# Kernel optimization log

Hardware: AMD Instinct MI355X
Metric: run time of the kernel (lower is better)

## Reference

```python
import jax, jax.numpy as jnp
import numpy as np

B, T, H = 2048, 784, 64
STATE_DIM = 1
IN_DIM = 1 + STATE_DIM  # concat([t, y])
INNER_LR = 0.01
NUM_GRAD_STEPS = 4


def _unif(k, shape, fan_in):
    lim = 1.0 / np.sqrt(fan_in)
    return jax.random.uniform(k, shape, jnp.float32, -lim, lim)


def setup_inputs() -> dict:
    key = jax.random.key(0)
    ks = jax.random.split(key, 8)
    ts = (jnp.arange(T, dtype=jnp.float32) / T)
    xs = jax.random.normal(ks[0], (B, T), jnp.float32)
    mask = jax.random.bernoulli(ks[1], 0.5, (B, T - 1))  # teacher-forcing draws
    # equinox Linear default init: U(-1/sqrt(fan_in), 1/sqrt(fan_in)) for W and b
    W1 = _unif(ks[2], (H, IN_DIM), IN_DIM)
    b1 = _unif(ks[3], (H,), IN_DIM)
    W2 = _unif(ks[4], (H, H), H)
    b2 = _unif(ks[5], (H,), H)
    W3 = _unif(ks[6], (STATE_DIM, H), H)
    b3 = _unif(ks[7], (STATE_DIM,), H)
    return {"ts": ts, "xs": xs, "mask": mask,
            "W1": W1, "b1": b1, "W2": W2, "b2": b2, "W3": W3, "b3": b3}


def _mlp(theta, t, y):
    # theta: tuple of (W1,b1,W2,b2,W3,b3); t, y scalars -> output (state_dim,)
    W1, b1, W2, b2, W3, b3 = theta
    h = jnp.stack([t, y])                # (2,)
    h = jnp.tanh(W1 @ h + b1)            # (H,)
    h = jnp.tanh(W2 @ h + b2)            # (H,)
    return W3 @ h + b3                   # (state_dim,)


def reference(ts, xs, mask, W1, b1, W2, b2, W3, b3):
    theta0 = (W1, b1, W2, b2, W3, b3)

    def forward(xs_row, mask_row):
        def step(carry, inp):
            theta, t_prev, x_hat, x_prev = carry
            x_true, t_curr, m = inp
            x_t = jnp.where(m, x_true, x_hat)  # bernoulli(0.5) teacher forcing

            def inner_loss(th):
                pred = _mlp(th, t_curr, x_prev)
                return jnp.mean((pred - x_t) ** 2)

            for _ in range(NUM_GRAD_STEPS):
                g = jax.grad(inner_loss)(theta)
                theta = jax.tree_util.tree_map(
                    lambda p, gr: p - INNER_LR * gr, theta, g)

            deltat = t_curr - t_prev
            x_hat_new = _mlp(theta, t_curr + deltat, x_true).squeeze()
            return (theta, t_curr, x_hat_new, x_true), x_hat_new

        init = (theta0, ts[0], xs_row[0], xs_row[0])
        _, x_hats = jax.lax.scan(step, init, (xs_row[1:], ts[1:], mask_row))
        return jnp.concatenate([xs_row[:1], x_hats], axis=0)  # (T,)

    return jax.vmap(forward)(xs, mask)  # (B, T)
```

## Files before the change

### kernel.cpp

```cpp
#include <hip/hip_runtime.h>
#include <math.h>


#define TT  784
#define HH  64
#define LR  0.01f

typedef _Float16 h2v __attribute__((ext_vector_type(2)));
#define FDOT2(a, b, c) __builtin_amdgcn_fdot2((a), (b), (c), false)
#define BC(f) __builtin_bit_cast(h2v, (f))
#define PKFMA(acc, a, b) acc = __builtin_elementwise_fma((a), (b), (acc))

__device__ __forceinline__ float fast_tanh(float x) {
    float e = __builtin_amdgcn_exp2f(x * 2.885390081777926814f);
    float r = __builtin_amdgcn_rcpf(e + 1.0f);
    return fmaf(-2.0f, r, 1.0f);
}

template <int CTRL, int RMASK, bool BC_>
__device__ __forceinline__ float dpp_add(float x) {
    int t = __builtin_amdgcn_update_dpp(0, __builtin_bit_cast(int, x),
                                        CTRL, RMASK, 0xf, BC_);
    return x + __builtin_bit_cast(float, t);
}

__device__ __forceinline__ float wave_sum(float x) {
    x = dpp_add<0x111, 0xf, true>(x);
    x = dpp_add<0x112, 0xf, true>(x);
    x = dpp_add<0x114, 0xf, true>(x);
    x = dpp_add<0x118, 0xf, true>(x);
    x = dpp_add<0x142, 0xa, false>(x);
    x = dpp_add<0x143, 0xc, false>(x);
    return __builtin_bit_cast(float,
        __builtin_amdgcn_readlane(__builtin_bit_cast(int, x), 63));
}

__global__ __launch_bounds__(64, 2)
void ttt_kernel(const float* __restrict__ ts,
                const float* __restrict__ xs,
                const int*   __restrict__ mask,
                const float* __restrict__ W1,
                const float* __restrict__ b1,
                const float* __restrict__ W2,
                const float* __restrict__ b2,
                const float* __restrict__ W3,
                const float* __restrict__ b3,
                float* __restrict__ out)
{
    __shared__ __align__(16) _Float16 s_h1h[HH];
    __shared__ __align__(16) _Float16 s_uh[HH];
    __shared__ float s_ts[TT];
    __shared__ float s_xs[TT];
    __shared__ float s_out[TT];
    __shared__ int   s_mask[TT - 1];

    const int row  = blockIdx.x;
    const int lane = threadIdx.x;

    for (int i = lane; i < TT; i += HH) {
        s_ts[i] = ts[i];
        s_xs[i] = xs[row * TT + i];
    }
    for (int i = lane; i < TT - 1; i += HH) s_mask[i] = mask[row * (TT - 1) + i];

    float w1a = W1[2 * lane + 0];
    float w1b = W1[2 * lane + 1];
    float b1v = b1[lane];
    float b2v = b2[lane];
    float w3v = W3[lane];
    float b3v = b3[0];

    h2v w2r[HH / 2];
    h2v w2c[HH / 2];
#pragma unroll
    for (int k = 0; k < HH / 2; ++k) {
        w2r[k] = h2v{(_Float16)W2[lane * HH + 2 * k], (_Float16)W2[lane * HH + 2 * k + 1]};
        w2c[k] = h2v{(_Float16)W2[(2 * k) * HH + lane], (_Float16)W2[(2 * k + 1) * HH + lane]};
    }
    __syncthreads();

    const float4* h1v4 = (const float4*)s_h1h;
    const float4* uv4  = (const float4*)s_uh;

    float t_prev = s_ts[0];
    const float x0 = s_xs[0];
    float x_hat  = x0;
    float x_prev = x0;
    if (lane == 0) s_out[0] = x0;

    float4 hr[8];
    float  h1f, h2f, predf;
    float  ul;
    float  z1f;
    float  sdz1 = 0.f;
    float  tc = 0.f, x_true = 0.f, tin = 0.f, nls = 0.f;

    auto MERGED = [&](float xt, bool final_) {
        const float diff = predf - xt;
        const float dl   = diff + diff;
        const float ndl  = -LR * dl;
        w3v = fmaf(ndl, h2f, w3v);
        b3v += ndl;
        b2v = fmaf(ndl, ul, b2v);
        const _Float16 sd = (_Float16)(ndl * ul);
        const h2v sdv = h2v{sd, sd};
        const _Float16 sh = (_Float16)(ndl * h1f);
        const h2v shv = h2v{sh, sh};
        float d0 = 0.f, d1 = 0.f, d2 = 0.f, d3 = 0.f;
#pragma unroll
        for (int k = 0; k < 8; ++k) {
            float4 q = uv4[k];
            d0 = FDOT2(w2c[4 * k + 0], BC(q.x), d0);
            d1 = FDOT2(w2c[4 * k + 1], BC(q.y), d1);
            d2 = FDOT2(w2c[4 * k + 2], BC(q.z), d2);
            d3 = FDOT2(w2c[4 * k + 3], BC(q.w), d3);
            PKFMA(w2c[4 * k + 0], shv, BC(q.x));
            PKFMA(w2c[4 * k + 1], shv, BC(q.y));
            PKFMA(w2c[4 * k + 2], shv, BC(q.z));
            PKFMA(w2c[4 * k + 3], shv, BC(q.w));
        }
        const float raw = (d0 + d1) + (d2 + d3);
        const float dh1 = dl * raw;
        const float dz1 = dh1 * fmaf(-h1f, h1f, 1.0f);
        sdz1 += dz1;
        if (!final_) {
            z1f = fmaf(nls, dz1, z1f);
        } else {
            w1a = fmaf(-LR * tc,     sdz1, w1a);
            w1b = fmaf(-LR * x_prev, sdz1, w1b);
            b1v = fmaf(-LR,          sdz1, b1v);
            z1f = fmaf(w1a, tin, fmaf(w1b, x_true, b1v));
        }
        h1f = fast_tanh(z1f);
        s_h1h[lane] = (_Float16)h1f;
#pragma unroll
        for (int k = 0; k < 8; ++k) {
            float4 o = hr[k];
            PKFMA(w2r[4 * k + 0], sdv, BC(o.x));
            PKFMA(w2r[4 * k + 1], sdv, BC(o.y));
            PKFMA(w2r[4 * k + 2], sdv, BC(o.z));
            PKFMA(w2r[4 * k + 3], sdv, BC(o.w));
        }
        float a0 = b2v, a1 = 0.f, a2 = 0.f, a3 = 0.f;
#pragma unroll
        for (int k = 0; k < 8; ++k) {
            float4 q = h1v4[k];
            hr[k] = q;
            a0 = FDOT2(w2r[4 * k + 0], BC(q.x), a0);
            a1 = FDOT2(w2r[4 * k + 1], BC(q.y), a1);
            a2 = FDOT2(w2r[4 * k + 2], BC(q.z), a2);
            a3 = FDOT2(w2r[4 * k + 3], BC(q.w), a3);
        }
        const float z2 = (a0 + a1) + (a2 + a3);
        h2f = fast_tanh(z2);
        const float uf = w3v * fmaf(-h2f, h2f, 1.0f);
        ul = uf;
        s_uh[lane] = (_Float16)uf;
        predf = wave_sum(w3v * h2f) + b3v;
    };

    z1f = fmaf(w1a, s_ts[1], fmaf(w1b, x0, b1v));
    h1f = fast_tanh(z1f);
    s_h1h[lane] = (_Float16)h1f;
    {
        float a0 = b2v, a1 = 0.f, a2 = 0.f, a3 = 0.f;
#pragma unroll
        for (int k = 0; k < 8; ++k) {
            float4 q = h1v4[k];
            hr[k] = q;
            a0 = FDOT2(w2r[4 * k + 0], BC(q.x), a0);
            a1 = FDOT2(w2r[4 * k + 1], BC(q.y), a1);
            a2 = FDOT2(w2r[4 * k + 2], BC(q.z), a2);
            a3 = FDOT2(w2r[4 * k + 3], BC(q.w), a3);
        }
        const float z2 = (a0 + a1) + (a2 + a3);
        h2f = fast_tanh(z2);
        const float uf = w3v * fmaf(-h2f, h2f, 1.0f);
        ul = uf;
        s_uh[lane] = (_Float16)uf;
        predf = wave_sum(w3v * h2f) + b3v;
    }

    for (int t = 1; t < TT; ++t) {
        tc     = s_ts[t];
        x_true = s_xs[t];
        tin    = tc + (tc - t_prev);
        nls    = -LR * fmaf(tc, tc, fmaf(x_prev, x_prev, 1.0f));
        const float x_t = s_mask[t - 1] ? x_true : x_hat;

        sdz1 = 0.f;
        MERGED(x_t, false);
        MERGED(x_t, false);
        MERGED(x_t, false);
        MERGED(x_t, true);
        x_hat = predf;

        if (lane == 0) s_out[t] = x_hat;
        t_prev = tc;
        x_prev = x_true;
    }

    for (int i = lane; i < TT; i += HH) out[row * TT + i] = s_out[i];
}

extern "C" void kernel_launch(void* const* d_in, const int* in_sizes, int n_in,
                              void* d_out, int out_size, void* d_ws, size_t ws_size,
                              hipStream_t stream) {
    const float* ts   = (const float*)d_in[0];
    const float* xs   = (const float*)d_in[1];
    const int*   mask = (const int*)d_in[2];
    const float* W1   = (const float*)d_in[3];
    const float* b1   = (const float*)d_in[4];
    const float* W2   = (const float*)d_in[5];
    const float* b2   = (const float*)d_in[6];
    const float* W3   = (const float*)d_in[7];
    const float* b3   = (const float*)d_in[8];
    float* out = (float*)d_out;

    const int B = in_sizes[1] / TT;
    dim3 grid(B), block(HH);
    hipLaunchKernelGGL(ttt_kernel, grid, block, 0, stream,
                       ts, xs, mask, W1, b1, W2, b2, W3, b3, out);
}
```

Baseline: 2.518 ms.

## Broadcast hidden vectors via DPP and readlane instead of LDS round-trips

Replaces the shared-memory staging of the fp16 h1 and u vectors with a DPP lane shift that packs neighbouring halves, followed by 32 readlanes into scalar/uniform registers. This removes LDS writes, reads and the implicit wait on them from the serial per-step dependency chain. It also folds the subtraction of x_t into the wave reduction by pre-dividing the bias term by 64, and splits the dot products into eight accumulators for more ILP. The cost is 64 readlane instructions per inner step and slightly different rounding in the loss gradient.

```diff
diff --git a/kernel.cpp b/kernel.cpp
--- a/kernel.cpp
+++ b/kernel.cpp
@@ -8,7 +8,7 @@
 
 typedef _Float16 h2v __attribute__((ext_vector_type(2)));
 #define FDOT2(a, b, c) __builtin_amdgcn_fdot2((a), (b), (c), false)
-#define BC(f) __builtin_bit_cast(h2v, (f))
+#define BCI(i) __builtin_bit_cast(h2v, (i))
 #define PKFMA(acc, a, b) acc = __builtin_elementwise_fma((a), (b), (acc))
 
 __device__ __forceinline__ float fast_tanh(float x) {
@@ -33,6 +33,10 @@
     x = dpp_add<0x143, 0xc, false>(x);
     return __builtin_bit_cast(float,
         __builtin_amdgcn_readlane(__builtin_bit_cast(int, x), 63));
+}
+
+__device__ __forceinline__ int lane_shl1(int v) {
+    return __builtin_amdgcn_update_dpp(0, v, 0x101, 0xf, 0xf, false);
 }
 
 __global__ __launch_bounds__(64, 2)
@@ -47,8 +51,6 @@
                 const float* __restrict__ b3,
                 float* __restrict__ out)
 {
-    __shared__ __align__(16) _Float16 s_h1h[HH];
-    __shared__ __align__(16) _Float16 s_uh[HH];
     __shared__ float s_ts[TT];
     __shared__ float s_xs[TT];
     __shared__ float s_out[TT];
@@ -79,26 +81,32 @@
     }
     __syncthreads();
 
-    const float4* h1v4 = (const float4*)s_h1h;
-    const float4* uv4  = (const float4*)s_uh;
-
     float t_prev = s_ts[0];
     const float x0 = s_xs[0];
     float x_hat  = x0;
     float x_prev = x0;
     if (lane == 0) s_out[0] = x0;
 
-    float4 hr[8];
+    int hb[32];
+    int ub[32];
     float  h1f, h2f, predf;
     float  ul;
     float  z1f;
     float  sdz1 = 0.f;
     float  tc = 0.f, x_true = 0.f, tin = 0.f, nls = 0.f;
 
-    auto MERGED = [&](float xt, bool final_) {
-        const float diff = predf - xt;
-        const float dl   = diff + diff;
-        const float ndl  = -LR * dl;
+    auto GATHER = [&](float x, int* dst) {
+        const int lo = (int)__builtin_bit_cast(unsigned short, (_Float16)x);
+        const int nb = lane_shl1(lo);
+        const int pk = lo | (nb << 16);
+#pragma unroll
+        for (int k = 0; k < 32; ++k)
+            dst[k] = __builtin_amdgcn_readlane(pk, 2 * k);
+    };
+
+    auto MERGED = [&](float diff, float xt, bool final_) -> float {
+        const float k12 = -2.0f * fmaf(h1f, h1f, -1.0f);
+        const float ndl = diff * (-2.0f * LR);
         w3v = fmaf(ndl, h2f, w3v);
         b3v += ndl;
         b2v = fmaf(ndl, ul, b2v);
@@ -107,21 +115,30 @@
         const _Float16 sh = (_Float16)(ndl * h1f);
         const h2v shv = h2v{sh, sh};
         float d0 = 0.f, d1 = 0.f, d2 = 0.f, d3 = 0.f;
+        float d4 = 0.f, d5 = 0.f, d6 = 0.f, d7 = 0.f;
 #pragma unroll
         for (int k = 0; k < 8; ++k) {
-            float4 q = uv4[k];
-            d0 = FDOT2(w2c[4 * k + 0], BC(q.x), d0);
-            d1 = FDOT2(w2c[4 * k + 1], BC(q.y), d1);
-            d2 = FDOT2(w2c[4 * k + 2], BC(q.z), d2);
-            d3 = FDOT2(w2c[4 * k + 3], BC(q.w), d3);
-            PKFMA(w2c[4 * k + 0], shv, BC(q.x));
-            PKFMA(w2c[4 * k + 1], shv, BC(q.y));
-            PKFMA(w2c[4 * k + 2], shv, BC(q.z));
-            PKFMA(w2c[4 * k + 3], shv, BC(q.w));
-        }
-        const float raw = (d0 + d1) + (d2 + d3);
-        const float dh1 = dl * raw;
-        const float dz1 = dh1 * fmaf(-h1f, h1f, 1.0f);
+            const h2v q0 = BCI(ub[4 * k + 0]), q1 = BCI(ub[4 * k + 1]);
+            const h2v q2 = BCI(ub[4 * k + 2]), q3 = BCI(ub[4 * k + 3]);
+            if (k & 1) {
+                d4 = FDOT2(w2c[4 * k + 0], q0, d4);
+                d5 = FDOT2(w2c[4 * k + 1], q1, d5);
+                d6 = FDOT2(w2c[4 * k + 2], q2, d6);
+                d7 = FDOT2(w2c[4 * k + 3], q3, d7);
+            } else {
+                d0 = FDOT2(w2c[4 * k + 0], q0, d0);
+                d1 = FDOT2(w2c[4 * k + 1], q1, d1);
+                d2 = FDOT2(w2c[4 * k + 2], q2, d2);
+                d3 = FDOT2(w2c[4 * k + 3], q3, d3);
+            }
+            PKFMA(w2c[4 * k + 0], shv, q0);
+            PKFMA(w2c[4 * k + 1], shv, q1);
+            PKFMA(w2c[4 * k + 2], shv, q2);
+            PKFMA(w2c[4 * k + 3], shv, q3);
+        }
+        const float raw = ((d0 + d4) + (d1 + d5)) + ((d2 + d6) + (d3 + d7));
+        const float rk2 = raw * k12;
+        const float dz1 = diff * rk2;
         sdz1 += dz1;
         if (!final_) {
             z1f = fmaf(nls, dz1, z1f);
@@ -132,53 +149,64 @@
             z1f = fmaf(w1a, tin, fmaf(w1b, x_true, b1v));
         }
         h1f = fast_tanh(z1f);
-        s_h1h[lane] = (_Float16)h1f;
+#pragma unroll
+        for (int k = 0; k < 32; ++k) PKFMA(w2r[k], sdv, BCI(hb[k]));
+        GATHER(h1f, hb);
+        float a0 = b2v, a1 = 0.f, a2 = 0.f, a3 = 0.f;
+        float a4 = 0.f, a5 = 0.f, a6 = 0.f, a7 = 0.f;
 #pragma unroll
         for (int k = 0; k < 8; ++k) {
-            float4 o = hr[k];
-            PKFMA(w2r[4 * k + 0], sdv, BC(o.x));
-            PKFMA(w2r[4 * k + 1], sdv, BC(o.y));
-            PKFMA(w2r[4 * k + 2], sdv, BC(o.z));
-            PKFMA(w2r[4 * k + 3], sdv, BC(o.w));
-        }
-        float a0 = b2v, a1 = 0.f, a2 = 0.f, a3 = 0.f;
-#pragma unroll
-        for (int k = 0; k < 8; ++k) {
-            float4 q = h1v4[k];
-            hr[k] = q;
-            a0 = FDOT2(w2r[4 * k + 0], BC(q.x), a0);
-            a1 = FDOT2(w2r[4 * k + 1], BC(q.y), a1);
-            a2 = FDOT2(w2r[4 * k + 2], BC(q.z), a2);
-            a3 = FDOT2(w2r[4 * k + 3], BC(q.w), a3);
-        }
-        const float z2 = (a0 + a1) + (a2 + a3);
+            const h2v q0 = BCI(hb[4 * k + 0]), q1 = BCI(hb[4 * k + 1]);
+            const h2v q2 = BCI(hb[4 * k + 2]), q3 = BCI(hb[4 * k + 3]);
+            if (k & 1) {
+                a4 = FDOT2(w2r[4 * k + 0], q0, a4);
+                a5 = FDOT2(w2r[4 * k + 1], q1, a5);
+                a6 = FDOT2(w2r[4 * k + 2], q2, a6);
+                a7 = FDOT2(w2r[4 * k + 3], q3, a7);
+            } else {
+                a0 = FDOT2(w2r[4 * k + 0], q0, a0);
+                a1 = FDOT2(w2r[4 * k + 1], q1, a1);
+                a2 = FDOT2(w2r[4 * k + 2], q2, a2);
+                a3 = FDOT2(w2r[4 * k + 3], q3, a3);
+            }
+        }
+        const float z2 = ((a0 + a4) + (a1 + a5)) + ((a2 + a6) + (a3 + a7));
         h2f = fast_tanh(z2);
         const float uf = w3v * fmaf(-h2f, h2f, 1.0f);
         ul = uf;
-        s_uh[lane] = (_Float16)uf;
-        predf = wave_sum(w3v * h2f) + b3v;
+        GATHER(uf, ub);
+        const float cadd = (final_ ? b3v : (b3v - xt)) * 0.015625f;
+        return wave_sum(fmaf(w3v, h2f, cadd));
     };
 
     z1f = fmaf(w1a, s_ts[1], fmaf(w1b, x0, b1v));
     h1f = fast_tanh(z1f);
-    s_h1h[lane] = (_Float16)h1f;
+    GATHER(h1f, hb);
     {
         float a0 = b2v, a1 = 0.f, a2 = 0.f, a3 = 0.f;
+        float a4 = 0.f, a5 = 0.f, a6 = 0.f, a7 = 0.f;
 #pragma unroll
         for (int k = 0; k < 8; ++k) {
-            float4 q = h1v4[k];
-            hr[k] = q;
-            a0 = FDOT2(w2r[4 * k + 0], BC(q.x), a0);
-            a1 = FDOT2(w2r[4 * k + 1], BC(q.y), a1);
-            a2 = FDOT2(w2r[4 * k + 2], BC(q.z), a2);
-            a3 = FDOT2(w2r[4 * k + 3], BC(q.w), a3);
-        }
-        const float z2 = (a0 + a1) + (a2 + a3);
+            const h2v q0 = BCI(hb[4 * k + 0]), q1 = BCI(hb[4 * k + 1]);
+            const h2v q2 = BCI(hb[4 * k + 2]), q3 = BCI(hb[4 * k + 3]);
+            if (k & 1) {
+                a4 = FDOT2(w2r[4 * k + 0], q0, a4);
+                a5 = FDOT2(w2r[4 * k + 1], q1, a5);
+                a6 = FDOT2(w2r[4 * k + 2], q2, a6);
+                a7 = FDOT2(w2r[4 * k + 3], q3, a7);
+            } else {
+                a0 = FDOT2(w2r[4 * k + 0], q0, a0);
+                a1 = FDOT2(w2r[4 * k + 1], q1, a1);
+                a2 = FDOT2(w2r[4 * k + 2], q2, a2);
+                a3 = FDOT2(w2r[4 * k + 3], q3, a3);
+            }
+        }
+        const float z2 = ((a0 + a4) + (a1 + a5)) + ((a2 + a6) + (a3 + a7));
         h2f = fast_tanh(z2);
         const float uf = w3v * fmaf(-h2f, h2f, 1.0f);
         ul = uf;
-        s_uh[lane] = (_Float16)uf;
-        predf = wave_sum(w3v * h2f) + b3v;
+        GATHER(uf, ub);
+        predf = wave_sum(fmaf(w3v, h2f, b3v * 0.015625f));
     }
 
     for (int t = 1; t < TT; ++t) {
@@ -189,10 +217,11 @@
         const float x_t = s_mask[t - 1] ? x_true : x_hat;
 
         sdz1 = 0.f;
-        MERGED(x_t, false);
-        MERGED(x_t, false);
-        MERGED(x_t, false);
-        MERGED(x_t, true);
+        float df = predf - x_t;
+        df    = MERGED(df, x_t, false);
+        df    = MERGED(df, x_t, false);
+        df    = MERGED(df, x_t, false);
+        predf = MERGED(df, x_t, true);
         x_hat = predf;
 
         if (lane == 0) s_out[t] = x_hat;
```

Result: slower. 3.244 ms (+28.8%).

## Switch W2 state from packed fp16 to fp32 with double-buffered LDS activations

Applied to the files above, without the earlier changes.

Replaces the packed half-precision W2 registers, fdot2 and packed-FMA updates with full fp32 weights and scalar FMAs. It also double-buffers the h1 activations in shared memory instead of caching the old h1 in registers for the rank-1 update. This roughly doubles the register footprint for W2 (128 floats per lane) and doubles the ALU instruction count in the inner loops. In exchange it removes fp16 rounding drift in the weights over many steps, with added risk of register spilling or lower occupancy.

```diff
diff --git a/kernel.cpp b/kernel.cpp
--- a/kernel.cpp
+++ b/kernel.cpp
@@ -5,11 +5,6 @@
 #define TT  784
 #define HH  64
 #define LR  0.01f
-
-typedef _Float16 h2v __attribute__((ext_vector_type(2)));
-#define FDOT2(a, b, c) __builtin_amdgcn_fdot2((a), (b), (c), false)
-#define BC(f) __builtin_bit_cast(h2v, (f))
-#define PKFMA(acc, a, b) acc = __builtin_elementwise_fma((a), (b), (acc))
 
 __device__ __forceinline__ float fast_tanh(float x) {
     float e = __builtin_amdgcn_exp2f(x * 2.885390081777926814f);
@@ -47,8 +42,8 @@
                 const float* __restrict__ b3,
                 float* __restrict__ out)
 {
-    __shared__ __align__(16) _Float16 s_h1h[HH];
-    __shared__ __align__(16) _Float16 s_uh[HH];
+    __shared__ __align__(16) float s_hb[2][HH];
+    __shared__ __align__(16) float s_ub[HH];
     __shared__ float s_ts[TT];
     __shared__ float s_xs[TT];
     __shared__ float s_out[TT];
@@ -70,17 +65,18 @@
     float w3v = W3[lane];
     float b3v = b3[0];
 
-    h2v w2r[HH / 2];
-    h2v w2c[HH / 2];
-#pragma unroll
-    for (int k = 0; k < HH / 2; ++k) {
-        w2r[k] = h2v{(_Float16)W2[lane * HH + 2 * k], (_Float16)W2[lane * HH + 2 * k + 1]};
-        w2c[k] = h2v{(_Float16)W2[(2 * k) * HH + lane], (_Float16)W2[(2 * k + 1) * HH + lane]};
+    float w2r[HH];
+    float w2c[HH];
+#pragma unroll
+    for (int j = 0; j < HH; ++j) {
+        w2r[j] = W2[lane * HH + j];
+        w2c[j] = W2[j * HH + lane];
     }
     __syncthreads();
 
-    const float4* h1v4 = (const float4*)s_h1h;
-    const float4* uv4  = (const float4*)s_uh;
+    const float4* hb0 = (const float4*)s_hb[0];
+    const float4* hb1 = (const float4*)s_hb[1];
+    const float4* ub4 = (const float4*)s_ub;
 
     float t_prev = s_ts[0];
     const float x0 = s_xs[0];
@@ -88,36 +84,34 @@
     float x_prev = x0;
     if (lane == 0) s_out[0] = x0;
 
-    float4 hr[8];
     float  h1f, h2f, predf;
     float  ul;
     float  z1f;
     float  sdz1 = 0.f;
     float  tc = 0.f, x_true = 0.f, tin = 0.f, nls = 0.f;
 
-    auto MERGED = [&](float xt, bool final_) {
+    auto MERGED = [&](const float4* hold, const float4* hnew, float* hst,
+                      float xt, bool final_) {
         const float diff = predf - xt;
         const float dl   = diff + diff;
         const float ndl  = -LR * dl;
         w3v = fmaf(ndl, h2f, w3v);
         b3v += ndl;
         b2v = fmaf(ndl, ul, b2v);
-        const _Float16 sd = (_Float16)(ndl * ul);
-        const h2v sdv = h2v{sd, sd};
-        const _Float16 sh = (_Float16)(ndl * h1f);
-        const h2v shv = h2v{sh, sh};
+        const float sd = ndl * ul;
+        const float sh = ndl * h1f;
         float d0 = 0.f, d1 = 0.f, d2 = 0.f, d3 = 0.f;
 #pragma unroll
-        for (int k = 0; k < 8; ++k) {
-            float4 q = uv4[k];
-            d0 = FDOT2(w2c[4 * k + 0], BC(q.x), d0);
-            d1 = FDOT2(w2c[4 * k + 1], BC(q.y), d1);
-            d2 = FDOT2(w2c[4 * k + 2], BC(q.z), d2);
-            d3 = FDOT2(w2c[4 * k + 3], BC(q.w), d3);
-            PKFMA(w2c[4 * k + 0], shv, BC(q.x));
-            PKFMA(w2c[4 * k + 1], shv, BC(q.y));
-            PKFMA(w2c[4 * k + 2], shv, BC(q.z));
-            PKFMA(w2c[4 * k + 3], shv, BC(q.w));
+        for (int k = 0; k < 16; ++k) {
+            const float4 q = ub4[k];
+            d0 = fmaf(w2c[4 * k + 0], q.x, d0);
+            d1 = fmaf(w2c[4 * k + 1], q.y, d1);
+            d2 = fmaf(w2c[4 * k + 2], q.z, d2);
+            d3 = fmaf(w2c[4 * k + 3], q.w, d3);
+            w2c[4 * k + 0] = fmaf(sh, q.x, w2c[4 * k + 0]);
+            w2c[4 * k + 1] = fmaf(sh, q.y, w2c[4 * k + 1]);
+            w2c[4 * k + 2] = fmaf(sh, q.z, w2c[4 * k + 2]);
+            w2c[4 * k + 3] = fmaf(sh, q.w, w2c[4 * k + 3]);
         }
         const float raw = (d0 + d1) + (d2 + d3);
         const float dh1 = dl * raw;
@@ -132,52 +126,47 @@
             z1f = fmaf(w1a, tin, fmaf(w1b, x_true, b1v));
         }
         h1f = fast_tanh(z1f);
-        s_h1h[lane] = (_Float16)h1f;
-#pragma unroll
-        for (int k = 0; k < 8; ++k) {
-            float4 o = hr[k];
-            PKFMA(w2r[4 * k + 0], sdv, BC(o.x));
-            PKFMA(w2r[4 * k + 1], sdv, BC(o.y));
-            PKFMA(w2r[4 * k + 2], sdv, BC(o.z));
-            PKFMA(w2r[4 * k + 3], sdv, BC(o.w));
-        }
+        hst[lane] = h1f;
         float a0 = b2v, a1 = 0.f, a2 = 0.f, a3 = 0.f;
 #pragma unroll
-        for (int k = 0; k < 8; ++k) {
-            float4 q = h1v4[k];
-            hr[k] = q;
-            a0 = FDOT2(w2r[4 * k + 0], BC(q.x), a0);
-            a1 = FDOT2(w2r[4 * k + 1], BC(q.y), a1);
-            a2 = FDOT2(w2r[4 * k + 2], BC(q.z), a2);
-            a3 = FDOT2(w2r[4 * k + 3], BC(q.w), a3);
+        for (int k = 0; k < 16; ++k) {
+            const float4 qo = hold[k];
+            w2r[4 * k + 0] = fmaf(sd, qo.x, w2r[4 * k + 0]);
+            w2r[4 * k + 1] = fmaf(sd, qo.y, w2r[4 * k + 1]);
+            w2r[4 * k + 2] = fmaf(sd, qo.z, w2r[4 * k + 2]);
+            w2r[4 * k + 3] = fmaf(sd, qo.w, w2r[4 * k + 3]);
+            const float4 qn = hnew[k];
+            a0 = fmaf(w2r[4 * k + 0], qn.x, a0);
+            a1 = fmaf(w2r[4 * k + 1], qn.y, a1);
+            a2 = fmaf(w2r[4 * k + 2], qn.z, a2);
+            a3 = fmaf(w2r[4 * k + 3], qn.w, a3);
         }
         const float z2 = (a0 + a1) + (a2 + a3);
         h2f = fast_tanh(z2);
         const float uf = w3v * fmaf(-h2f, h2f, 1.0f);
         ul = uf;
-        s_uh[lane] = (_Float16)uf;
+        s_ub[lane] = uf;
         predf = wave_sum(w3v * h2f) + b3v;
     };
 
     z1f = fmaf(w1a, s_ts[1], fmaf(w1b, x0, b1v));
     h1f = fast_tanh(z1f);
-    s_h1h[lane] = (_Float16)h1f;
+    s_hb[0][lane] = h1f;
     {
         float a0 = b2v, a1 = 0.f, a2 = 0.f, a3 = 0.f;
 #pragma unroll
-        for (int k = 0; k < 8; ++k) {
-            float4 q = h1v4[k];
-            hr[k] = q;
-            a0 = FDOT2(w2r[4 * k + 0], BC(q.x), a0);
-            a1 = FDOT2(w2r[4 * k + 1], BC(q.y), a1);
-            a2 = FDOT2(w2r[4 * k + 2], BC(q.z), a2);
-            a3 = FDOT2(w2r[4 * k + 3], BC(q.w), a3);
+        for (int k = 0; k < 16; ++k) {
+            const float4 qn = hb0[k];
+            a0 = fmaf(w2r[4 * k + 0], qn.x, a0);
+            a1 = fmaf(w2r[4 * k + 1], qn.y, a1);
+            a2 = fmaf(w2r[4 * k + 2], qn.z, a2);
+            a3 = fmaf(w2r[4 * k + 3], qn.w, a3);
         }
         const float z2 = (a0 + a1) + (a2 + a3);
         h2f = fast_tanh(z2);
         const float uf = w3v * fmaf(-h2f, h2f, 1.0f);
         ul = uf;
-        s_uh[lane] = (_Float16)uf;
+        s_ub[lane] = uf;
         predf = wave_sum(w3v * h2f) + b3v;
     }
 
@@ -189,10 +178,10 @@
         const float x_t = s_mask[t - 1] ? x_true : x_hat;
 
         sdz1 = 0.f;
-        MERGED(x_t, false);
-        MERGED(x_t, false);
-        MERGED(x_t, false);
-        MERGED(x_t, true);
+        MERGED(hb0, hb1, s_hb[1], x_t, false);
+        MERGED(hb1, hb0, s_hb[0], x_t, false);
+        MERGED(hb0, hb1, s_hb[1], x_t, false);
+        MERGED(hb1, hb0, s_hb[0], x_t, true);
         x_hat = predf;
 
         if (lane == 0) s_out[t] = x_hat;
```

Result: slower. 5.411 ms (+114.9%).
